# Kernel optimization log

Measured on AMD Instinct MI355X. Metric: run time of the kernel, lower is better.

Reference implementation:

```python
import jax, jax.numpy as jnp
import numpy as np

N_ITERS = 10
ETA = 0.1


def setup_inputs() -> dict:
    key = jax.random.key(0)
    k1, k2, k3 = jax.random.split(key, 3)
    u = jax.random.normal(k1, (65536, 512), dtype=jnp.float32)
    G_raw = jax.random.normal(k2, (512, 512), dtype=jnp.float32) * 0.01
    # log_lam initialized as log(0.5), matching lam_init=0.5
    log_lam = jnp.asarray(np.log(0.5), dtype=jnp.float32)
    return {"u": u, "G_raw": G_raw, "log_lam": log_lam}


def reference(u, G_raw, log_lam):
    lam = jnp.exp(log_lam)
    # symmetrize and zero the diagonal
    G = 0.5 * (G_raw + G_raw.T)
    G = G - jnp.diag(jnp.diagonal(G))

    def step(carry, _):
        v, a = carry
        dv = u - v - a @ G          # [N, dim]
        v = v + ETA * dv
        a = jnp.sign(v) * jax.nn.relu(jnp.abs(v) - lam)  # soft threshold
        return (v, a), None

    init = (jnp.zeros_like(u), jnp.zeros_like(u))
    (v, a), _ = jax.lax.scan(step, init, None, length=N_ITERS)
    return a
```

## Files before the change

### kernel.cpp

```cpp
#include <hip/hip_runtime.h>
#include <hip/hip_bf16.h>


typedef __attribute__((ext_vector_type(8))) short bf16x8;
typedef __attribute__((ext_vector_type(16))) float f32x16;

#define ETA 0.1f

__device__ __forceinline__ unsigned short f2bf(float f) {
  union { float f; unsigned u; } x; x.f = f;
  unsigned r = x.u + 0x7fffu + ((x.u >> 16) & 1u);
  return (unsigned short)(r >> 16);
}

__global__ void prep_G(const float* __restrict__ Graw, unsigned short* __restrict__ Gb) {
  int idx = blockIdx.x * blockDim.x + threadIdx.x;
  int k = idx >> 9, n = idx & 511;
  float g = 0.5f * (Graw[k * 512 + n] + Graw[n * 512 + k]);
  if (k == n) g = 0.f;
  int kk = k >> 4, ct = n >> 5;
  int lane = (n & 31) + (((k >> 3) & 1) << 5);
  int j = k & 7;
  Gb[((((kk * 16 + ct) * 64) + lane) << 3) + j] = f2bf(g);
}

__global__ __launch_bounds__(512, 2) void lca_kernel(
    const float* __restrict__ u_g, const unsigned short* __restrict__ Gb,
    const float* __restrict__ log_lam, float* __restrict__ out) {
  __shared__ unsigned short sA[2][64 * 520];

  const int tid = threadIdx.x;
  const int lane = tid & 63;
  const int wave = tid >> 6;
  const int R0 = blockIdx.x * 64;
  const int cl = lane & 31;
  const int rquad = (lane >> 5) * 4;
  const int C0 = wave * 64;
  const int s = (blockIdx.x >> 3) & 31;

  const float lam = expf(log_lam[0]);

  f32x16 acc[2][2];
  f32x16 uu[2][2];

  #pragma unroll
  for (int rt = 0; rt < 2; ++rt) {
    #pragma unroll
    for (int ctl = 0; ctl < 2; ++ctl) {
      const int lrow = rt * 32 + rquad;
      const int gcol = C0 + ctl * 32 + cl;
      const float* ub = u_g + (R0 + lrow) * 512 + gcol;
      unsigned short* sa = &sA[0][lrow * 520 + gcol];
      #pragma unroll
      for (int reg = 0; reg < 16; ++reg) {
        const int rofs = (reg & 3) + 8 * (reg >> 2);
        float uv = ub[rofs * 512];
        uu[rt][ctl][reg] = uv;
        float v = ETA * uv;
        float av = copysignf(fmaxf(fabsf(v) - lam, 0.f), v);
        sa[rofs * 520] = f2bf(av);
        acc[rt][ctl][reg] = -1.9f * uv;
      }
    }
  }

  const bf16x8* gb = (const bf16x8*)Gb;
  const int bb = (wave * 2) * 64 + lane;

  bf16x8 p0a = gb[bb + ((s + 0) & 31) * 1024], p0b = gb[bb + ((s + 0) & 31) * 1024 + 64];
  bf16x8 p1a = gb[bb + ((s + 1) & 31) * 1024], p1b = gb[bb + ((s + 1) & 31) * 1024 + 64];
  bf16x8 p2a = gb[bb + ((s + 2) & 31) * 1024], p2b = gb[bb + ((s + 2) & 31) * 1024 + 64];
  bf16x8 p3a = gb[bb + ((s + 3) & 31) * 1024], p3b = gb[bb + ((s + 3) & 31) * 1024 + 64];

  __syncthreads();

  auto epilogue = [&](unsigned short* sbuf) {
    #pragma unroll
    for (int rt = 0; rt < 2; ++rt) {
      #pragma unroll
      for (int ctl = 0; ctl < 2; ++ctl) {
        unsigned short* sa = &sbuf[(rt * 32 + rquad) * 520 + C0 + ctl * 32 + cl];
        #pragma unroll
        for (int reg = 0; reg < 16; ++reg) {
          const int rofs = (reg & 3) + 8 * (reg >> 2);
          float v = -ETA * acc[rt][ctl][reg];
          float av = copysignf(fmaxf(fabsf(v) - lam, 0.f), v);
          sa[rofs * 520] = f2bf(av);
          acc[rt][ctl][reg] = 0.9f * acc[rt][ctl][reg] - uu[rt][ctl][reg];
        }
      }
    }
  };

#define STEP(KBASE, J, PA, PB)                                                   \
  do {                                                                           \
    const int kc = ((KBASE) + (J) + s) & 31;                                     \
    const int kl = ((KBASE) + (J) + 4 + s) & 31;                                 \
    bf16x8 a0 = *(const bf16x8*)(paRow + kc * 16);                               \
    bf16x8 a1 = *(const bf16x8*)(paRow + 32 * 520 + kc * 16);                    \
    __builtin_amdgcn_s_setprio(1);                                               \
    acc[0][0] = __builtin_amdgcn_mfma_f32_32x32x16_bf16(a0, PA, acc[0][0], 0, 0, 0); \
    acc[0][1] = __builtin_amdgcn_mfma_f32_32x32x16_bf16(a0, PB, acc[0][1], 0, 0, 0); \
    acc[1][0] = __builtin_amdgcn_mfma_f32_32x32x16_bf16(a1, PA, acc[1][0], 0, 0, 0); \
    acc[1][1] = __builtin_amdgcn_mfma_f32_32x32x16_bf16(a1, PB, acc[1][1], 0, 0, 0); \
    __builtin_amdgcn_s_setprio(0);                                               \
    PA = gb[bb + kl * 1024];                                                     \
    PB = gb[bb + kl * 1024 + 64];                                                \
  } while (0)

  #pragma unroll 1
  for (int t = 1; t < 10; ++t) {
    const unsigned short* paRow = sA[(t + 1) & 1] + cl * 520 + ((lane >> 5) << 3);
    #pragma unroll 1
    for (int grp = 0; grp < 8; ++grp) {
      const int k4 = grp * 4;
      STEP(k4, 0, p0a, p0b);
      STEP(k4, 1, p1a, p1b);
      STEP(k4, 2, p2a, p2b);
      STEP(k4, 3, p3a, p3b);
    }
    if (t < 9) {
      epilogue(sA[t & 1]);
      __syncthreads();
    }
  }
#undef STEP

  #pragma unroll
  for (int rt = 0; rt < 2; ++rt) {
    #pragma unroll
    for (int ctl = 0; ctl < 2; ++ctl) {
      float* ob = out + (R0 + rt * 32 + rquad) * 512 + C0 + ctl * 32 + cl;
      #pragma unroll
      for (int reg = 0; reg < 16; ++reg) {
        const int rofs = (reg & 3) + 8 * (reg >> 2);
        float v = -ETA * acc[rt][ctl][reg];
        ob[rofs * 512] = copysignf(fmaxf(fabsf(v) - lam, 0.f), v);
      }
    }
  }
}

extern "C" void kernel_launch(void* const* d_in, const int* in_sizes, int n_in,
                              void* d_out, int out_size, void* d_ws, size_t ws_size,
                              hipStream_t stream) {
  const float* u = (const float*)d_in[0];
  const float* Graw = (const float*)d_in[1];
  const float* log_lam = (const float*)d_in[2];
  float* out = (float*)d_out;
  unsigned short* Gb = (unsigned short*)d_ws;

  prep_G<<<dim3(1024), dim3(256), 0, stream>>>(Graw, Gb);
  lca_kernel<<<dim3(1024), dim3(512), 0, stream>>>(u, Gb, log_lam, out);
}
```

Before: 476.6 us.

## Template row tiles per block, single-buffer LDS, split launch into 96- and 64-row kernels

The kernel is templated on the number of 32-row tiles per block. The main launch uses 96-row blocks (3 tiles) over the first 49152 rows, and a second launch with 64-row blocks covers the remaining 16384. The LDS activation buffer goes from double-buffered to a single buffer with an extra barrier before the epilogue overwrites it, and the G prefetch depth drops from 4 to 2 register sets. The aim is more reuse of each G fragment across rows and fewer register/LDS resources per block, at the cost of an added sync per iteration and a second kernel launch that may tail poorly.

```diff
diff --git a/kernel.cpp b/kernel.cpp
--- a/kernel.cpp
+++ b/kernel.cpp
@@ -24,15 +24,16 @@
   Gb[((((kk * 16 + ct) * 64) + lane) << 3) + j] = f2bf(g);
 }
 
+template <int NRT>
 __global__ __launch_bounds__(512, 2) void lca_kernel(
     const float* __restrict__ u_g, const unsigned short* __restrict__ Gb,
-    const float* __restrict__ log_lam, float* __restrict__ out) {
-  __shared__ unsigned short sA[2][64 * 520];
+    const float* __restrict__ log_lam, float* __restrict__ out, int row_base) {
+  __shared__ unsigned short sA[NRT * 32 * 520];
 
   const int tid = threadIdx.x;
   const int lane = tid & 63;
   const int wave = tid >> 6;
-  const int R0 = blockIdx.x * 64;
+  const int R0 = row_base + blockIdx.x * (NRT * 32);
   const int cl = lane & 31;
   const int rquad = (lane >> 5) * 4;
   const int C0 = wave * 64;
@@ -40,17 +41,17 @@
 
   const float lam = expf(log_lam[0]);
 
-  f32x16 acc[2][2];
-  f32x16 uu[2][2];
+  f32x16 acc[NRT][2];
+  f32x16 uu[NRT][2];
 
   #pragma unroll
-  for (int rt = 0; rt < 2; ++rt) {
+  for (int rt = 0; rt < NRT; ++rt) {
     #pragma unroll
     for (int ctl = 0; ctl < 2; ++ctl) {
       const int lrow = rt * 32 + rquad;
       const int gcol = C0 + ctl * 32 + cl;
       const float* ub = u_g + (R0 + lrow) * 512 + gcol;
-      unsigned short* sa = &sA[0][lrow * 520 + gcol];
+      unsigned short* sa = &sA[lrow * 520 + gcol];
       #pragma unroll
       for (int reg = 0; reg < 16; ++reg) {
         const int rofs = (reg & 3) + 8 * (reg >> 2);
@@ -67,42 +68,27 @@
   const bf16x8* gb = (const bf16x8*)Gb;
   const int bb = (wave * 2) * 64 + lane;
 
-  bf16x8 p0a = gb[bb + ((s + 0) & 31) * 1024], p0b = gb[bb + ((s + 0) & 31) * 1024 + 64];
-  bf16x8 p1a = gb[bb + ((s + 1) & 31) * 1024], p1b = gb[bb + ((s + 1) & 31) * 1024 + 64];
-  bf16x8 p2a = gb[bb + ((s + 2) & 31) * 1024], p2b = gb[bb + ((s + 2) & 31) * 1024 + 64];
-  bf16x8 p3a = gb[bb + ((s + 3) & 31) * 1024], p3b = gb[bb + ((s + 3) & 31) * 1024 + 64];
+  bf16x8 P0a = gb[bb + ((s + 0) & 31) * 1024], P0b = gb[bb + ((s + 0) & 31) * 1024 + 64];
+  bf16x8 P1a = gb[bb + ((s + 1) & 31) * 1024], P1b = gb[bb + ((s + 1) & 31) * 1024 + 64];
 
   __syncthreads();
 
-  auto epilogue = [&](unsigned short* sbuf) {
-    #pragma unroll
-    for (int rt = 0; rt < 2; ++rt) {
-      #pragma unroll
-      for (int ctl = 0; ctl < 2; ++ctl) {
-        unsigned short* sa = &sbuf[(rt * 32 + rquad) * 520 + C0 + ctl * 32 + cl];
-        #pragma unroll
-        for (int reg = 0; reg < 16; ++reg) {
-          const int rofs = (reg & 3) + 8 * (reg >> 2);
-          float v = -ETA * acc[rt][ctl][reg];
-          float av = copysignf(fmaxf(fabsf(v) - lam, 0.f), v);
-          sa[rofs * 520] = f2bf(av);
-          acc[rt][ctl][reg] = 0.9f * acc[rt][ctl][reg] - uu[rt][ctl][reg];
-        }
-      }
-    }
-  };
+  const unsigned short* paRow = sA + cl * 520 + ((lane >> 5) << 3);
 
-#define STEP(KBASE, J, PA, PB)                                                   \
+#define STEP(KK, PA, PB)                                                         \
   do {                                                                           \
-    const int kc = ((KBASE) + (J) + s) & 31;                                     \
-    const int kl = ((KBASE) + (J) + 4 + s) & 31;                                 \
-    bf16x8 a0 = *(const bf16x8*)(paRow + kc * 16);                               \
-    bf16x8 a1 = *(const bf16x8*)(paRow + 32 * 520 + kc * 16);                    \
+    const int kc = ((KK) + s) & 31;                                              \
+    const int kl = ((KK) + 2 + s) & 31;                                          \
+    bf16x8 a_[NRT];                                                              \
+    _Pragma("unroll")                                                            \
+    for (int rt = 0; rt < NRT; ++rt)                                             \
+      a_[rt] = *(const bf16x8*)(paRow + rt * (32 * 520) + kc * 16);              \
     __builtin_amdgcn_s_setprio(1);                                               \
-    acc[0][0] = __builtin_amdgcn_mfma_f32_32x32x16_bf16(a0, PA, acc[0][0], 0, 0, 0); \
-    acc[0][1] = __builtin_amdgcn_mfma_f32_32x32x16_bf16(a0, PB, acc[0][1], 0, 0, 0); \
-    acc[1][0] = __builtin_amdgcn_mfma_f32_32x32x16_bf16(a1, PA, acc[1][0], 0, 0, 0); \
-    acc[1][1] = __builtin_amdgcn_mfma_f32_32x32x16_bf16(a1, PB, acc[1][1], 0, 0, 0); \
+    _Pragma("unroll")                                                            \
+    for (int rt = 0; rt < NRT; ++rt) {                                           \
+      acc[rt][0] = __builtin_amdgcn_mfma_f32_32x32x16_bf16(a_[rt], PA, acc[rt][0], 0, 0, 0); \
+      acc[rt][1] = __builtin_amdgcn_mfma_f32_32x32x16_bf16(a_[rt], PB, acc[rt][1], 0, 0, 0); \
+    }                                                                            \
     __builtin_amdgcn_s_setprio(0);                                               \
     PA = gb[bb + kl * 1024];                                                     \
     PB = gb[bb + kl * 1024 + 64];                                                \
@@ -110,24 +96,35 @@
 
   #pragma unroll 1
   for (int t = 1; t < 10; ++t) {
-    const unsigned short* paRow = sA[(t + 1) & 1] + cl * 520 + ((lane >> 5) << 3);
     #pragma unroll 1
-    for (int grp = 0; grp < 8; ++grp) {
-      const int k4 = grp * 4;
-      STEP(k4, 0, p0a, p0b);
-      STEP(k4, 1, p1a, p1b);
-      STEP(k4, 2, p2a, p2b);
-      STEP(k4, 3, p3a, p3b);
+    for (int kk = 0; kk < 32; kk += 2) {
+      STEP(kk, P0a, P0b);
+      STEP(kk + 1, P1a, P1b);
     }
+    __syncthreads();
     if (t < 9) {
-      epilogue(sA[t & 1]);
+      #pragma unroll
+      for (int rt = 0; rt < NRT; ++rt) {
+        #pragma unroll
+        for (int ctl = 0; ctl < 2; ++ctl) {
+          unsigned short* sa = &sA[(rt * 32 + rquad) * 520 + C0 + ctl * 32 + cl];
+          #pragma unroll
+          for (int reg = 0; reg < 16; ++reg) {
+            const int rofs = (reg & 3) + 8 * (reg >> 2);
+            float v = -ETA * acc[rt][ctl][reg];
+            float av = copysignf(fmaxf(fabsf(v) - lam, 0.f), v);
+            sa[rofs * 520] = f2bf(av);
+            acc[rt][ctl][reg] = 0.9f * acc[rt][ctl][reg] - uu[rt][ctl][reg];
+          }
+        }
+      }
       __syncthreads();
     }
   }
 #undef STEP
 
   #pragma unroll
-  for (int rt = 0; rt < 2; ++rt) {
+  for (int rt = 0; rt < NRT; ++rt) {
     #pragma unroll
     for (int ctl = 0; ctl < 2; ++ctl) {
       float* ob = out + (R0 + rt * 32 + rquad) * 512 + C0 + ctl * 32 + cl;
@@ -151,5 +148,6 @@
   unsigned short* Gb = (unsigned short*)d_ws;
 
   prep_G<<<dim3(1024), dim3(256), 0, stream>>>(Graw, Gb);
-  lca_kernel<<<dim3(1024), dim3(512), 0, stream>>>(u, Gb, log_lam, out);
+  lca_kernel<3><<<dim3(512), dim3(512), 0, stream>>>(u, Gb, log_lam, out, 0);
+  lca_kernel<2><<<dim3(256), dim3(512), 0, stream>>>(u, Gb, log_lam, out, 512 * 96);
 }
```

Measured after the change: 475.5 us. About the same (-0.2%).
